# Kernel tuning notes

Hardware: AMD Instinct MI355X
Metric: run time of the kernel (lower is better)

The kernel has to match this reference:

```python
import jax, jax.numpy as jnp
import numpy as np

B, T, C = 2, 4096, 768
H = 12
D = C // H  # head_dim = 64

def setup_inputs() -> dict:
    key = jax.random.key(0)
    ks = jax.random.split(key, 5)
    s = 1.0 / np.sqrt(C)
    return {
        "x": jax.random.normal(ks[0], (B, T, C), dtype=jnp.float32),
        "qkv_w": jax.random.normal(ks[1], (C, 3 * C), dtype=jnp.float32) * s,
        "qkv_b": jax.random.normal(ks[2], (3 * C,), dtype=jnp.float32) * 0.02,
        "out_w": jax.random.normal(ks[3], (C, C), dtype=jnp.float32) * s,
        "out_b": jax.random.normal(ks[4], (C,), dtype=jnp.float32) * 0.02,
    }

def reference(x, qkv_w, qkv_b, out_w, out_b):
    b, t, c = x.shape
    qkv = x @ qkv_w + qkv_b                      # [B,T,3C]
    q, k, v = jnp.split(qkv, 3, axis=-1)
    # [B,T,C] -> [B,H,T,D]
    q = q.reshape(b, t, H, D).transpose(0, 2, 1, 3)
    k = k.reshape(b, t, H, D).transpose(0, 2, 1, 3)
    v = v.reshape(b, t, H, D).transpose(0, 2, 1, 3)
    scale = 1.0 / np.sqrt(D)
    attn = jnp.einsum('bhqd,bhkd->bhqk', q, k) * scale  # [B,H,T,T]
    causal = jnp.tril(jnp.ones((t, t), dtype=bool))
    attn = jnp.where(causal, attn, -jnp.inf)
    attn = jax.nn.softmax(attn, axis=-1)
    y = jnp.einsum('bhqk,bhkd->bhqd', attn, v)           # [B,H,T,D]
    y = y.transpose(0, 2, 1, 3).reshape(b, t, c)
    return y @ out_w + out_b
```

## Files before the change

### kernel.cpp

```cpp
#include <hip/hip_runtime.h>
#include <hip/hip_bf16.h>

#define T_SEQ 4096
#define C_DIM 768
#define H_NUM 12
#define D_HEAD 64
#define N3    2304
#define BHN   24

typedef __bf16 bf16x8 __attribute__((ext_vector_type(8)));
typedef float  f32x4  __attribute__((ext_vector_type(4)));

__device__ inline unsigned short f2b(float f) {
    unsigned int x = __float_as_uint(f);
    unsigned int r = (x + 0x7FFFu + ((x >> 16) & 1u)) >> 16;
    return (unsigned short)r;
}

__device__ inline unsigned int pack_trunc(float lo, float hi) {
    return __builtin_amdgcn_perm(__float_as_uint(hi), __float_as_uint(lo), 0x07060302u);
}

__device__ inline void load_lds16(const unsigned short* g, unsigned short* l) {
    __builtin_amdgcn_global_load_lds(
        (const __attribute__((address_space(1))) unsigned int*)(g),
        (__attribute__((address_space(3))) unsigned int*)(l),
        16, 0, 0);
}

__device__ inline void transpose_tile(const float* __restrict__ in,
                                      unsigned short* __restrict__ out,
                                      unsigned short* Ts, int k0, int n0,
                                      int R, int Cc, int tid)
{
    #pragma unroll
    for (int it = 0; it < 4; ++it) {
        int idx = tid + it * 256;
        int r = idx >> 4, c4 = idx & 15;
        float4 v = *reinterpret_cast<const float4*>(&in[(size_t)(k0 + r) * Cc + n0 + c4 * 4]);
        Ts[(c4 * 4 + 0) * 72 + r] = f2b(v.x);
        Ts[(c4 * 4 + 1) * 72 + r] = f2b(v.y);
        Ts[(c4 * 4 + 2) * 72 + r] = f2b(v.z);
        Ts[(c4 * 4 + 3) * 72 + r] = f2b(v.w);
    }
    __syncthreads();
    #pragma unroll
    for (int it = 0; it < 2; ++it) {
        int idx = tid + it * 256;
        int row = idx >> 3, ch = idx & 7;
        *reinterpret_cast<uint4*>(&out[(size_t)(n0 + row) * R + k0 + ch * 8]) =
            *reinterpret_cast<const uint4*>(&Ts[row * 72 + ch * 8]);
    }
}

__global__ __launch_bounds__(256) void prep(
    const float* __restrict__ x, const float* __restrict__ qkv_w,
    const float* __restrict__ out_w,
    unsigned short* __restrict__ xb, unsigned short* __restrict__ wtq,
    unsigned short* __restrict__ wto)
{
    __shared__ unsigned short Ts[64 * 72];
    const int b = blockIdx.x, tid = threadIdx.x;
    if (b < 6144) {
        int idx = b * 256 + tid;
        float4 v = reinterpret_cast<const float4*>(x)[idx];
        ushort4 u;
        u.x = f2b(v.x); u.y = f2b(v.y); u.z = f2b(v.z); u.w = f2b(v.w);
        reinterpret_cast<ushort4*>(xb)[idx] = u;
    } else if (b < 6576) {
        int bb = b - 6144;
        transpose_tile(qkv_w, wtq, Ts, (bb % 12) * 64, (bb / 12) * 64, C_DIM, N3, tid);
    } else {
        int bb = b - 6576;
        transpose_tile(out_w, wto, Ts, (bb % 12) * 64, (bb / 12) * 64, C_DIM, C_DIM, tid);
    }
}

__global__ __launch_bounds__(256) void qkv_gemm(
    const unsigned short* __restrict__ xb, const unsigned short* __restrict__ wt,
    const float* __restrict__ bias,
    unsigned short* __restrict__ Q, unsigned short* __restrict__ K,
    unsigned short* __restrict__ Vt)
{
    __shared__ unsigned short SH[128 * 128];
    unsigned short* As = SH;
    unsigned short* Bs = SH + 128 * 64;
    const int tid  = threadIdx.x;
    const int m0   = blockIdx.x * 128;
    const int n0   = blockIdx.y * 128;
    const int lane = tid & 63;
    const int wv   = tid >> 6;
    const int wr   = wv >> 1, wc = wv & 1;
    const int quad = lane >> 4;
    const int lr   = lane & 15;
    const int srow = lane >> 3;
    const int dch  = (lane & 7) ^ srow;

    f32x4 acc[4][4] = {};

    for (int kk = 0; kk < C_DIM; kk += 64) {
        __syncthreads();
        #pragma unroll
        for (int i = 0; i < 4; ++i) {
            int inst = wv * 4 + i;
            int r = inst * 8 + srow;
            load_lds16(xb + (size_t)(m0 + r) * C_DIM + kk + dch * 8, As + inst * 512);
            load_lds16(wt + (size_t)(n0 + r) * C_DIM + kk + dch * 8, Bs + inst * 512);
        }
        __syncthreads();
        #pragma unroll
        for (int k2 = 0; k2 < 2; ++k2) {
            bf16x8 af[4], bf[4];
            #pragma unroll
            for (int mt = 0; mt < 4; ++mt)
                af[mt] = *reinterpret_cast<const bf16x8*>(
                    &As[(wr * 64 + mt * 16 + lr) * 64 + (((k2 * 4 + quad) ^ (lr & 7)) * 8)]);
            #pragma unroll
            for (int nt = 0; nt < 4; ++nt)
                bf[nt] = *reinterpret_cast<const bf16x8*>(
                    &Bs[(wc * 64 + nt * 16 + lr) * 64 + (((k2 * 4 + quad) ^ (lr & 7)) * 8)]);
            #pragma unroll
            for (int mt = 0; mt < 4; ++mt)
                #pragma unroll
                for (int nt = 0; nt < 4; ++nt)
                    acc[mt][nt] = __builtin_amdgcn_mfma_f32_16x16x32_bf16(af[mt], bf[nt], acc[mt][nt], 0, 0, 0);
        }
    }

    const int whichblk = n0 / C_DIM;
    if (whichblk == 2) {
        __syncthreads();
        #pragma unroll
        for (int nt = 0; nt < 4; ++nt) {
            int dp = wc * 64 + nt * 16 + lr;
            float bj = bias[n0 + dp];
            #pragma unroll
            for (int mt = 0; mt < 4; ++mt) {
                int t0 = wr * 64 + mt * 16 + quad * 4;
                ushort4 u;
                u.x = f2b(acc[mt][nt][0] + bj);
                u.y = f2b(acc[mt][nt][1] + bj);
                u.z = f2b(acc[mt][nt][2] + bj);
                u.w = f2b(acc[mt][nt][3] + bj);
                int cs = (t0 >> 2) ^ ((dp & 15) << 1);
                *reinterpret_cast<ushort4*>(&SH[dp * 128 + cs * 4]) = u;
            }
        }
        __syncthreads();
        const int bb = m0 >> 12;
        const int t_base = m0 & 4095;
        const int h_base = (n0 - 2 * C_DIM) >> 6;
        #pragma unroll
        for (int i = 0; i < 8; ++i) {
            int idx = i * 256 + tid;
            int row = idx >> 4, cc = idx & 15;
            int pc = ((2 * cc) ^ ((row & 15) << 1)) * 4;
            uint4 val = *reinterpret_cast<const uint4*>(&SH[row * 128 + pc]);
            int head = h_base + (row >> 6);
            int d = row & 63;
            *reinterpret_cast<uint4*>(
                &Vt[((size_t)(bb * H_NUM + head) * D_HEAD + d) * T_SEQ + t_base + cc * 8]) = val;
        }
    } else {
        const int head0 = ((n0 % C_DIM) + wc * 64) >> 6;
        #pragma unroll
        for (int nt = 0; nt < 4; ++nt) {
            int d = nt * 16 + lr;
            float bj = bias[n0 + wc * 64 + nt * 16 + lr];
            #pragma unroll
            for (int mt = 0; mt < 4; ++mt) {
                #pragma unroll
                for (int reg = 0; reg < 4; ++reg) {
                    int i = m0 + wr * 64 + mt * 16 + quad * 4 + reg;
                    int bb = i >> 12, t = i & 4095;
                    float val = acc[mt][nt][reg] + bj;
                    size_t base = (size_t)(bb * H_NUM + head0) * T_SEQ + t;
                    if (whichblk == 0)
                        Q[base * D_HEAD + d] = f2b(val * 0.18033688011f);
                    else
                        K[base * D_HEAD + d] = f2b(val);
                }
            }
        }
    }
}

__global__ __launch_bounds__(256, 3) void flash_attn(
    const unsigned short* __restrict__ Q, const unsigned short* __restrict__ K,
    const unsigned short* __restrict__ Vt, unsigned short* __restrict__ Y,
    float* __restrict__ pO, float* __restrict__ pl)
{
    __shared__ unsigned short Ks[2][64 * 64];
    __shared__ unsigned short Vs[2][64 * 64];
    __shared__ unsigned short Ps[2][64 * 72];
    const int tid  = threadIdx.x;
    const int lane = tid & 63;
    const int wv   = tid >> 6;
    const int quad = lane >> 4;
    const int lr   = lane & 15;
    const int srow = lane >> 3;
    const int dch  = (lane & 7) ^ srow;

    const int bid = blockIdx.x;
    const int ip  = bid / BHN;
    const int bh  = bid % BHN;

    const unsigned short* Qb = Q  + (size_t)bh * T_SEQ * D_HEAD;
    const unsigned short* Kb = K  + (size_t)bh * T_SEQ * D_HEAD;
    const unsigned short* Vb = Vt + (size_t)bh * D_HEAD * T_SEQ;

    int njob, jqt[2], jk0[2], jk1[2], jpart[2];
    if (ip < 16) {
        njob = 2;
        jqt[0] = ip;      jk0[0] = 0; jk1[0] = 2 * ip + 2;  jpart[0] = 0;
        jqt[1] = 31 - ip; jk0[1] = 0; jk1[1] = 31 - 2 * ip; jpart[1] = 1;
    } else {
        njob = 1;
        jqt[0] = ip; jk0[0] = 2 * ip - 31; jk1[0] = 2 * ip + 2; jpart[0] = 2;
    }

    bf16x8 ones;
    #pragma unroll
    for (int i = 0; i < 8; ++i) ones[i] = (__bf16)1.0f;
    const f32x4 zf = {};

    unsigned short* Pw0 = &Ps[0][(wv * 16) * 72];
    unsigned short* Pw1 = &Ps[1][(wv * 16) * 72];
    const int bb = bh / H_NUM, hh = bh % H_NUM;

    int buf = 0;
    {
        int kt = jk0[0];
        #pragma unroll
        for (int i = 0; i < 2; ++i) {
            int inst = wv * 2 + i;
            int r = inst * 8 + srow;
            load_lds16(Kb + (size_t)(kt * 64 + r) * D_HEAD + dch * 8, Ks[0] + inst * 512);
            load_lds16(Vb + (size_t)r * T_SEQ + kt * 64 + dch * 8, Vs[0] + inst * 512);
        }
    }

    for (int job = 0; job < njob; ++job) {
        const int qt = jqt[job];
        const int q0 = qt * 128;
        const int diag0 = 2 * qt;
        const int lastk = 2 * qt + 1;
        const int k0 = jk0[job], k1 = jk1[job];

        bf16x8 bQ[2][2];
        #pragma unroll
        for (int h = 0; h < 2; ++h)
            #pragma unroll
            for (int k2 = 0; k2 < 2; ++k2)
                bQ[h][k2] = *reinterpret_cast<const bf16x8*>(
                    &Qb[(size_t)(q0 + h * 64 + wv * 16 + lr) * D_HEAD + k2 * 32 + quad * 8]);

        f32x4 oacc[2][4] = {};
        f32x4 lacc[2] = {};

        for (int kt = k0; kt < k1; ++kt) {
            __syncthreads();

            int nkt = (kt + 1 < k1) ? (kt + 1) : ((job + 1 < njob) ? jk0[job + 1] : -1);
            if (nkt >= 0) {
                #pragma unroll
                for (int i = 0; i < 2; ++i) {
                    int inst = wv * 2 + i;
                    int r = inst * 8 + srow;
                    load_lds16(Kb + (size_t)(nkt * 64 + r) * D_HEAD + dch * 8,
                               Ks[buf ^ 1] + inst * 512);
                    load_lds16(Vb + (size_t)r * T_SEQ + nkt * 64 + dch * 8,
                               Vs[buf ^ 1] + inst * 512);
                }
            }

            const bool doh0 = (kt <= diag0);

            bf16x8 aK[4][2];
            #pragma unroll
            for (int mt = 0; mt < 4; ++mt)
                #pragma unroll
                for (int k2 = 0; k2 < 2; ++k2)
                    aK[mt][k2] = *reinterpret_cast<const bf16x8*>(
                        &Ks[buf][(mt * 16 + lr) * 64 + (((k2 * 4 + quad) ^ (lr & 7)) * 8)]);

            f32x4 st0[4], st1[4];
            #pragma unroll
            for (int mt = 0; mt < 4; ++mt) {
                st1[mt] = __builtin_amdgcn_mfma_f32_16x16x32_bf16(aK[mt][0], bQ[1][0], zf, 0, 0, 0);
                st1[mt] = __builtin_amdgcn_mfma_f32_16x16x32_bf16(aK[mt][1], bQ[1][1], st1[mt], 0, 0, 0);
            }
            if (doh0) {
                #pragma unroll
                for (int mt = 0; mt < 4; ++mt) {
                    st0[mt] = __builtin_amdgcn_mfma_f32_16x16x32_bf16(aK[mt][0], bQ[0][0], zf, 0, 0, 0);
                    st0[mt] = __builtin_amdgcn_mfma_f32_16x16x32_bf16(aK[mt][1], bQ[0][1], st0[mt], 0, 0, 0);
                }
            }

            if (kt == diag0) {
                int qg = q0 + wv * 16 + lr;
                #pragma unroll
                for (int mt = 0; mt < 4; ++mt)
                    #pragma unroll
                    for (int reg = 0; reg < 4; ++reg)
                        if (kt * 64 + mt * 16 + quad * 4 + reg > qg) st0[mt][reg] = -INFINITY;
            }
            if (kt == lastk) {
                int qg = q0 + 64 + wv * 16 + lr;
                #pragma unroll
                for (int mt = 0; mt < 4; ++mt)
                    #pragma unroll
                    for (int reg = 0; reg < 4; ++reg)
                        if (kt * 64 + mt * 16 + quad * 4 + reg > qg) st1[mt][reg] = -INFINITY;
            }

            #pragma unroll
            for (int mt = 0; mt < 4; ++mt) {
                #pragma unroll
                for (int reg = 0; reg < 4; ++reg)
                    st1[mt][reg] = __builtin_amdgcn_exp2f(st1[mt][reg]);
                uint2 u;
                u.x = pack_trunc(st1[mt][0], st1[mt][1]);
                u.y = pack_trunc(st1[mt][2], st1[mt][3]);
                *reinterpret_cast<uint2*>(&Pw1[lr * 72 + mt * 16 + quad * 4]) = u;
            }
            if (doh0) {
                #pragma unroll
                for (int mt = 0; mt < 4; ++mt) {
                    #pragma unroll
                    for (int reg = 0; reg < 4; ++reg)
                        st0[mt][reg] = __builtin_amdgcn_exp2f(st0[mt][reg]);
                    uint2 u;
                    u.x = pack_trunc(st0[mt][0], st0[mt][1]);
                    u.y = pack_trunc(st0[mt][2], st0[mt][3]);
                    *reinterpret_cast<uint2*>(&Pw0[lr * 72 + mt * 16 + quad * 4]) = u;
                }
            }

            bf16x8 aV[4][2];
            #pragma unroll
            for (int mt = 0; mt < 4; ++mt)
                #pragma unroll
                for (int k2 = 0; k2 < 2; ++k2)
                    aV[mt][k2] = *reinterpret_cast<const bf16x8*>(
                        &Vs[buf][(mt * 16 + lr) * 64 + (((k2 * 4 + quad) ^ (lr & 7)) * 8)]);

            if (doh0) {
                bf16x8 bP0 = *reinterpret_cast<const bf16x8*>(&Pw0[lr * 72 + quad * 8]);
                bf16x8 bP1 = *reinterpret_cast<const bf16x8*>(&Pw0[lr * 72 + 32 + quad * 8]);
                #pragma unroll
                for (int dt = 0; dt < 4; ++dt) {
                    oacc[0][dt] = __builtin_amdgcn_mfma_f32_16x16x32_bf16(aV[dt][0], bP0, oacc[0][dt], 0, 0, 0);
                    oacc[0][dt] = __builtin_amdgcn_mfma_f32_16x16x32_bf16(aV[dt][1], bP1, oacc[0][dt], 0, 0, 0);
                }
                lacc[0] = __builtin_amdgcn_mfma_f32_16x16x32_bf16(ones, bP0, lacc[0], 0, 0, 0);
                lacc[0] = __builtin_amdgcn_mfma_f32_16x16x32_bf16(ones, bP1, lacc[0], 0, 0, 0);
            }
            {
                bf16x8 bP0 = *reinterpret_cast<const bf16x8*>(&Pw1[lr * 72 + quad * 8]);
                bf16x8 bP1 = *reinterpret_cast<const bf16x8*>(&Pw1[lr * 72 + 32 + quad * 8]);
                #pragma unroll
                for (int dt = 0; dt < 4; ++dt) {
                    oacc[1][dt] = __builtin_amdgcn_mfma_f32_16x16x32_bf16(aV[dt][0], bP0, oacc[1][dt], 0, 0, 0);
                    oacc[1][dt] = __builtin_amdgcn_mfma_f32_16x16x32_bf16(aV[dt][1], bP1, oacc[1][dt], 0, 0, 0);
                }
                lacc[1] = __builtin_amdgcn_mfma_f32_16x16x32_bf16(ones, bP0, lacc[1], 0, 0, 0);
                lacc[1] = __builtin_amdgcn_mfma_f32_16x16x32_bf16(ones, bP1, lacc[1], 0, 0, 0);
            }

            buf ^= 1;
        }

        if (jpart[job] == 0) {
            #pragma unroll
            for (int h = 0; h < 2; ++h) {
                float inv = 1.f / lacc[h][0];
                int q = q0 + h * 64 + wv * 16 + lr;
                #pragma unroll
                for (int dt = 0; dt < 4; ++dt) {
                    ushort4 u;
                    u.x = f2b(oacc[h][dt][0] * inv);
                    u.y = f2b(oacc[h][dt][1] * inv);
                    u.z = f2b(oacc[h][dt][2] * inv);
                    u.w = f2b(oacc[h][dt][3] * inv);
                    *reinterpret_cast<ushort4*>(
                        &Y[(size_t)(bb * T_SEQ + q) * C_DIM + hh * 64 + dt * 16 + quad * 4]) = u;
                }
            }
        } else {
            const int slot = jpart[job] - 1;
            const int iH = 31 - qt;
            const size_t s = (size_t)slot * 384 + (size_t)bh * 16 + iH;
            float* po  = pO + s * 8192;
            float* plp = pl + s * 128;
            #pragma unroll
            for (int h = 0; h < 2; ++h) {
                int q = h * 64 + wv * 16 + lr;
                if (quad == 0) plp[q] = lacc[h][0];
                #pragma unroll
                for (int dt = 0; dt < 4; ++dt)
                    *reinterpret_cast<f32x4*>(&po[(size_t)q * 64 + dt * 16 + quad * 4]) = oacc[h][dt];
            }
        }
    }
}

__global__ __launch_bounds__(256) void combine(
    const float* __restrict__ pO, const float* __restrict__ pl,
    unsigned short* __restrict__ Y)
{
    const int s   = blockIdx.x;
    const int tid = threadIdx.x;
    const int bh  = s / 16, iH = s % 16;
    const int qt  = 31 - iH;
    const int bb  = bh / H_NUM, hh = bh % H_NUM;
    const int q0  = qt * 128;
    const float* a  = pO + (size_t)s * 8192;
    const float* b  = pO + (size_t)(384 + s) * 8192;
    const float* la = pl + (size_t)s * 128;
    const float* lb = pl + (size_t)(384 + s) * 128;
    #pragma unroll
    for (int j = 0; j < 8; ++j) {
        int idx = tid + j * 256;
        int f = idx * 4;
        int q = f >> 6, d0 = f & 63;
        float4 va = *reinterpret_cast<const float4*>(&a[f]);
        float4 vb = *reinterpret_cast<const float4*>(&b[f]);
        float inv = 1.f / (la[q] + lb[q]);
        ushort4 u;
        u.x = f2b((va.x + vb.x) * inv);
        u.y = f2b((va.y + vb.y) * inv);
        u.z = f2b((va.z + vb.z) * inv);
        u.w = f2b((va.w + vb.w) * inv);
        *reinterpret_cast<ushort4*>(
            &Y[(size_t)(bb * T_SEQ + q0 + q) * C_DIM + hh * 64 + d0]) = u;
    }
}

__global__ __launch_bounds__(256) void out_gemm(
    const unsigned short* __restrict__ Y, const unsigned short* __restrict__ wt,
    const float* __restrict__ bias, float* __restrict__ out)
{
    __shared__ unsigned short As[128 * 64];
    __shared__ unsigned short Bs[64 * 64];
    const int tid  = threadIdx.x;
    const int m0   = blockIdx.x * 128;
    const int n0   = blockIdx.y * 64;
    const int lane = tid & 63;
    const int wv   = tid >> 6;
    const int wr   = wv >> 1, wc = wv & 1;
    const int quad = lane >> 4;
    const int lr   = lane & 15;
    const int srow = lane >> 3;
    const int dch  = (lane & 7) ^ srow;

    f32x4 acc[4][2] = {};

    for (int kk = 0; kk < C_DIM; kk += 64) {
        __syncthreads();
        #pragma unroll
        for (int i = 0; i < 4; ++i) {
            int inst = wv * 4 + i;
            int r = inst * 8 + srow;
            load_lds16(Y + (size_t)(m0 + r) * C_DIM + kk + dch * 8, As + inst * 512);
        }
        #pragma unroll
        for (int i = 0; i < 2; ++i) {
            int inst = wv * 2 + i;
            int r = inst * 8 + srow;
            load_lds16(wt + (size_t)(n0 + r) * C_DIM + kk + dch * 8, Bs + inst * 512);
        }
        __syncthreads();
        #pragma unroll
        for (int k2 = 0; k2 < 2; ++k2) {
            bf16x8 af[4], bf[2];
            #pragma unroll
            for (int mt = 0; mt < 4; ++mt)
                af[mt] = *reinterpret_cast<const bf16x8*>(
                    &As[(wr * 64 + mt * 16 + lr) * 64 + (((k2 * 4 + quad) ^ (lr & 7)) * 8)]);
            #pragma unroll
            for (int nt = 0; nt < 2; ++nt)
                bf[nt] = *reinterpret_cast<const bf16x8*>(
                    &Bs[(wc * 32 + nt * 16 + lr) * 64 + (((k2 * 4 + quad) ^ (lr & 7)) * 8)]);
            #pragma unroll
            for (int mt = 0; mt < 4; ++mt)
                #pragma unroll
                for (int nt = 0; nt < 2; ++nt)
                    acc[mt][nt] = __builtin_amdgcn_mfma_f32_16x16x32_bf16(af[mt], bf[nt], acc[mt][nt], 0, 0, 0);
        }
    }

    #pragma unroll
    for (int nt = 0; nt < 2; ++nt) {
        int j = n0 + wc * 32 + nt * 16 + lr;
        float bj = bias[j];
        #pragma unroll
        for (int mt = 0; mt < 4; ++mt)
            #pragma unroll
            for (int reg = 0; reg < 4; ++reg) {
                int i = m0 + wr * 64 + mt * 16 + quad * 4 + reg;
                out[(size_t)i * C_DIM + j] = acc[mt][nt][reg] + bj;
            }
    }
}

extern "C" void kernel_launch(void* const* d_in, const int* in_sizes, int n_in,
                              void* d_out, int out_size, void* d_ws, size_t ws_size,
                              hipStream_t stream) {
    const float* x     = (const float*)d_in[0];
    const float* qkv_w = (const float*)d_in[1];
    const float* qkv_b = (const float*)d_in[2];
    const float* out_w = (const float*)d_in[3];
    const float* out_b = (const float*)d_in[4];
    float* out = (float*)d_out;

    unsigned short* xb  = (unsigned short*)d_ws;
    unsigned short* wtq = xb  + (size_t)8192 * 768;
    unsigned short* wto = wtq + (size_t)2304 * 768;
    unsigned short* Qs  = wto + (size_t)768 * 768;
    unsigned short* Kg  = Qs  + (size_t)BHN * T_SEQ * D_HEAD;
    unsigned short* Vt  = Kg  + (size_t)BHN * T_SEQ * D_HEAD;
    float*          pO  = (float*)(Vt + (size_t)BHN * T_SEQ * D_HEAD);
    float*          pl  = pO + (size_t)2 * 384 * 8192;
    unsigned short* Y   = xb;

    prep      <<<6720, 256, 0, stream>>>(x, qkv_w, out_w, xb, wtq, wto);
    qkv_gemm  <<<dim3(64, 18), 256, 0, stream>>>(xb, wtq, qkv_b, Qs, Kg, Vt);
    flash_attn<<<dim3(32 * BHN), 256, 0, stream>>>(Qs, Kg, Vt, Y, pO, pl);
    combine   <<<384, 256, 0, stream>>>(pO, pl, Y);
    out_gemm  <<<dim3(64, 12), 256, 0, stream>>>(Y, wto, out_b, out);
}
```

Before: 224.8 us.

## Keep softmax P in registers by permuting V's key order, dropping LDS round-trip

The exponentiated score tile P is no longer written to shared memory and read back as an MFMA operand. It is packed directly from the S accumulator registers into the bf16x8 B-operand. For this to be correct, the key ordering inside each 64-key tile of the transposed V is permuted when the QKV projection writes Vt, so the V operand's k-index matches the register layout of P. This removes the per-iteration LDS stores and loads for P and frees the Ps shared buffer, which may improve occupancy. In exchange, the Vt write now uses two 8-byte LDS reads instead of one 16-byte read.

```diff
diff --git a/kernel.cpp b/kernel.cpp
--- a/kernel.cpp
+++ b/kernel.cpp
@@ -10,6 +10,7 @@
 
 typedef __bf16 bf16x8 __attribute__((ext_vector_type(8)));
 typedef float  f32x4  __attribute__((ext_vector_type(4)));
+typedef unsigned int u32x4v __attribute__((ext_vector_type(4)));
 
 __device__ inline unsigned short f2b(float f) {
     unsigned int x = __float_as_uint(f);
@@ -154,12 +155,17 @@
         for (int i = 0; i < 8; ++i) {
             int idx = i * 256 + tid;
             int row = idx >> 4, cc = idx & 15;
-            int pc = ((2 * cc) ^ ((row & 15) << 1)) * 4;
-            uint4 val = *reinterpret_cast<const uint4*>(&SH[row * 128 + pc]);
+            int tile = cc >> 3, cp = cc & 7;
+            int G0 = tile * 16 + ((cp >> 2) << 3) + (cp & 3);
+            int swz = (row & 15) << 1;
+            uint2 lo = *reinterpret_cast<const uint2*>(&SH[row * 128 + ((G0 ^ swz) * 4)]);
+            uint2 hi = *reinterpret_cast<const uint2*>(&SH[row * 128 + (((G0 + 4) ^ swz) * 4)]);
+            uint4 val = {lo.x, lo.y, hi.x, hi.y};
             int head = h_base + (row >> 6);
             int d = row & 63;
             *reinterpret_cast<uint4*>(
-                &Vt[((size_t)(bb * H_NUM + head) * D_HEAD + d) * T_SEQ + t_base + cc * 8]) = val;
+                &Vt[((size_t)(bb * H_NUM + head) * D_HEAD + d) * T_SEQ +
+                    t_base + tile * 64 + cp * 8]) = val;
         }
     } else {
         const int head0 = ((n0 % C_DIM) + wc * 64) >> 6;
@@ -192,7 +198,6 @@
 {
     __shared__ unsigned short Ks[2][64 * 64];
     __shared__ unsigned short Vs[2][64 * 64];
-    __shared__ unsigned short Ps[2][64 * 72];
     const int tid  = threadIdx.x;
     const int lane = tid & 63;
     const int wv   = tid >> 6;
@@ -224,8 +229,6 @@
     for (int i = 0; i < 8; ++i) ones[i] = (__bf16)1.0f;
     const f32x4 zf = {};
 
-    unsigned short* Pw0 = &Ps[0][(wv * 16) * 72];
-    unsigned short* Pw1 = &Ps[1][(wv * 16) * 72];
     const int bb = bh / H_NUM, hh = bh % H_NUM;
 
     int buf = 0;
@@ -298,6 +301,14 @@
                 }
             }
 
+            bf16x8 aV[4][2];
+            #pragma unroll
+            for (int dt = 0; dt < 4; ++dt)
+                #pragma unroll
+                for (int f = 0; f < 2; ++f)
+                    aV[dt][f] = *reinterpret_cast<const bf16x8*>(
+                        &Vs[buf][(dt * 16 + lr) * 64 + (((f * 4 + quad) ^ (lr & 7)) * 8)]);
+
             if (kt == diag0) {
                 int qg = q0 + wv * 16 + lr;
                 #pragma unroll
@@ -315,58 +326,61 @@
                         if (kt * 64 + mt * 16 + quad * 4 + reg > qg) st1[mt][reg] = -INFINITY;
             }
 
-            #pragma unroll
-            for (int mt = 0; mt < 4; ++mt) {
-                #pragma unroll
-                for (int reg = 0; reg < 4; ++reg)
-                    st1[mt][reg] = __builtin_amdgcn_exp2f(st1[mt][reg]);
-                uint2 u;
-                u.x = pack_trunc(st1[mt][0], st1[mt][1]);
-                u.y = pack_trunc(st1[mt][2], st1[mt][3]);
-                *reinterpret_cast<uint2*>(&Pw1[lr * 72 + mt * 16 + quad * 4]) = u;
+            bf16x8 bP1a, bP1b, bP0a, bP0b;
+            {
+                #pragma unroll
+                for (int mt = 0; mt < 4; ++mt)
+                    #pragma unroll
+                    for (int reg = 0; reg < 4; ++reg)
+                        st1[mt][reg] = __builtin_amdgcn_exp2f(st1[mt][reg]);
+                u32x4v u;
+                u[0] = pack_trunc(st1[0][0], st1[0][1]);
+                u[1] = pack_trunc(st1[0][2], st1[0][3]);
+                u[2] = pack_trunc(st1[1][0], st1[1][1]);
+                u[3] = pack_trunc(st1[1][2], st1[1][3]);
+                bP1a = __builtin_bit_cast(bf16x8, u);
+                u[0] = pack_trunc(st1[2][0], st1[2][1]);
+                u[1] = pack_trunc(st1[2][2], st1[2][3]);
+                u[2] = pack_trunc(st1[3][0], st1[3][1]);
+                u[3] = pack_trunc(st1[3][2], st1[3][3]);
+                bP1b = __builtin_bit_cast(bf16x8, u);
             }
             if (doh0) {
                 #pragma unroll
-                for (int mt = 0; mt < 4; ++mt) {
+                for (int mt = 0; mt < 4; ++mt)
                     #pragma unroll
                     for (int reg = 0; reg < 4; ++reg)
                         st0[mt][reg] = __builtin_amdgcn_exp2f(st0[mt][reg]);
-                    uint2 u;
-                    u.x = pack_trunc(st0[mt][0], st0[mt][1]);
-                    u.y = pack_trunc(st0[mt][2], st0[mt][3]);
-                    *reinterpret_cast<uint2*>(&Pw0[lr * 72 + mt * 16 + quad * 4]) = u;
+                u32x4v u;
+                u[0] = pack_trunc(st0[0][0], st0[0][1]);
+                u[1] = pack_trunc(st0[0][2], st0[0][3]);
+                u[2] = pack_trunc(st0[1][0], st0[1][1]);
+                u[3] = pack_trunc(st0[1][2], st0[1][3]);
+                bP0a = __builtin_bit_cast(bf16x8, u);
+                u[0] = pack_trunc(st0[2][0], st0[2][1]);
+                u[1] = pack_trunc(st0[2][2], st0[2][3]);
+                u[2] = pack_trunc(st0[3][0], st0[3][1]);
+                u[3] = pack_trunc(st0[3][2], st0[3][3]);
+                bP0b = __builtin_bit_cast(bf16x8, u);
+            }
+
+            if (doh0) {
+                #pragma unroll
+                for (int dt = 0; dt < 4; ++dt) {
+                    oacc[0][dt] = __builtin_amdgcn_mfma_f32_16x16x32_bf16(aV[dt][0], bP0a, oacc[0][dt], 0, 0, 0);
+                    oacc[0][dt] = __builtin_amdgcn_mfma_f32_16x16x32_bf16(aV[dt][1], bP0b, oacc[0][dt], 0, 0, 0);
                 }
-            }
-
-            bf16x8 aV[4][2];
-            #pragma unroll
-            for (int mt = 0; mt < 4; ++mt)
-                #pragma unroll
-                for (int k2 = 0; k2 < 2; ++k2)
-                    aV[mt][k2] = *reinterpret_cast<const bf16x8*>(
-                        &Vs[buf][(mt * 16 + lr) * 64 + (((k2 * 4 + quad) ^ (lr & 7)) * 8)]);
-
-            if (doh0) {
-                bf16x8 bP0 = *reinterpret_cast<const bf16x8*>(&Pw0[lr * 72 + quad * 8]);
-                bf16x8 bP1 = *reinterpret_cast<const bf16x8*>(&Pw0[lr * 72 + 32 + quad * 8]);
+                lacc[0] = __builtin_amdgcn_mfma_f32_16x16x32_bf16(ones, bP0a, lacc[0], 0, 0, 0);
+                lacc[0] = __builtin_amdgcn_mfma_f32_16x16x32_bf16(ones, bP0b, lacc[0], 0, 0, 0);
+            }
+            {
                 #pragma unroll
                 for (int dt = 0; dt < 4; ++dt) {
-                    oacc[0][dt] = __builtin_amdgcn_mfma_f32_16x16x32_bf16(aV[dt][0], bP0, oacc[0][dt], 0, 0, 0);
-                    oacc[0][dt] = __builtin_amdgcn_mfma_f32_16x16x32_bf16(aV[dt][1], bP1, oacc[0][dt], 0, 0, 0);
+                    oacc[1][dt] = __builtin_amdgcn_mfma_f32_16x16x32_bf16(aV[dt][0], bP1a, oacc[1][dt], 0, 0, 0);
+                    oacc[1][dt] = __builtin_amdgcn_mfma_f32_16x16x32_bf16(aV[dt][1], bP1b, oacc[1][dt], 0, 0, 0);
                 }
-                lacc[0] = __builtin_amdgcn_mfma_f32_16x16x32_bf16(ones, bP0, lacc[0], 0, 0, 0);
-                lacc[0] = __builtin_amdgcn_mfma_f32_16x16x32_bf16(ones, bP1, lacc[0], 0, 0, 0);
-            }
-            {
-                bf16x8 bP0 = *reinterpret_cast<const bf16x8*>(&Pw1[lr * 72 + quad * 8]);
-                bf16x8 bP1 = *reinterpret_cast<const bf16x8*>(&Pw1[lr * 72 + 32 + quad * 8]);
-                #pragma unroll
-                for (int dt = 0; dt < 4; ++dt) {
-                    oacc[1][dt] = __builtin_amdgcn_mfma_f32_16x16x32_bf16(aV[dt][0], bP0, oacc[1][dt], 0, 0, 0);
-                    oacc[1][dt] = __builtin_amdgcn_mfma_f32_16x16x32_bf16(aV[dt][1], bP1, oacc[1][dt], 0, 0, 0);
-                }
-                lacc[1] = __builtin_amdgcn_mfma_f32_16x16x32_bf16(ones, bP0, lacc[1], 0, 0, 0);
-                lacc[1] = __builtin_amdgcn_mfma_f32_16x16x32_bf16(ones, bP1, lacc[1], 0, 0, 0);
+                lacc[1] = __builtin_amdgcn_mfma_f32_16x16x32_bf16(ones, bP1a, lacc[1], 0, 0, 0);
+                lacc[1] = __builtin_amdgcn_mfma_f32_16x16x32_bf16(ones, bP1b, lacc[1], 0, 0, 0);
             }
 
             buf ^= 1;
```

Measured after the change: 218.6 us. 2.8% less time.
